# Performance work log

Measured on AMD Instinct MI355X. Metric: run time of the kernel, lower is better.

The kernel has to match this reference:

```python
import jax, jax.numpy as jnp
import numpy as np
import math

HID = 1024      # opt.hidden_dim
NH = 8          # num_heads (hardcoded in module)
HD = HID // NH  # indiv_head_dim = 128
G = 16          # opt.group_num
GD = HID // G   # per-group dim = 64
FEAT = 1024     # opt.feature_dim
V, T = 8, 256   # videos x frames
E = 256         # number of events
L = 64          # max_att_len (clip window)
N = 384         # expanded event_num
WAVE = 10000.0


def setup_inputs() -> dict:
    rng = np.random.RandomState(0)
    key = jax.random.key(0)
    ks = jax.random.split(key, 12)

    feats = jax.random.normal(ks[0], (V * T, FEAT), dtype=jnp.float32)

    # ragged clip spans -> dense gather idx + mask (the Basic_Encoder loop)
    starts = rng.randint(0, V * T - L, size=(E,))
    clip_gather_idx = jnp.asarray(starts[:, None] + np.arange(L)[None, :], dtype=jnp.int32)
    lens = rng.randint(8, L + 1, size=(E,))
    clip_mask = jnp.asarray((np.arange(L)[None, :] < lens[:, None]).astype(np.float32))

    # event_seq_idx expansion: rows -> event ids, block-diagonal mask
    expand_idx = jnp.asarray(rng.randint(0, E, size=(N,)), dtype=jnp.int32)
    block_mask = np.zeros((N, N), dtype=np.float32)
    pos = 0
    while pos < N:
        b = min(int(rng.randint(8, 49)), N - pos)
        block_mask[pos:pos + b, pos:pos + b] = 1.0
        pos += b
    block_mask = jnp.asarray(block_mask)

    # normalized timestamps (start < end, in [0,1])
    s = rng.uniform(0.0, 0.8, size=(N, 1)).astype(np.float32)
    e = s + rng.uniform(0.02, 0.2, size=(N, 1)).astype(np.float32)
    bbox = jnp.asarray(np.concatenate([s, e], axis=1))

    sc = 1.0 / math.sqrt(HID)
    scd = 1.0 / math.sqrt(HD)
    Wpre = jax.random.normal(ks[1], (HID, FEAT), dtype=jnp.float32) * sc
    bpre = jnp.zeros((HID,), dtype=jnp.float32)
    Wq = jax.random.normal(ks[2], (NH, HD, HD), dtype=jnp.float32) * scd
    bq = jnp.zeros((NH, HD), dtype=jnp.float32)
    Wk = jax.random.normal(ks[3], (NH, HD, HD), dtype=jnp.float32) * scd
    bk = jnp.zeros((NH, HD), dtype=jnp.float32)
    Wv = jax.random.normal(ks[4], (NH, HD, HD), dtype=jnp.float32) * scd
    bv = jnp.zeros((NH, HD), dtype=jnp.float32)
    Wp1 = jax.random.normal(ks[5], (HID, HID), dtype=jnp.float32) * sc
    bp1 = jnp.zeros((HID,), dtype=jnp.float32)
    Wp2 = jax.random.normal(ks[6], (G, HID), dtype=jnp.float32) * sc
    bp2 = jnp.zeros((G,), dtype=jnp.float32)

    return dict(feats=feats, clip_gather_idx=clip_gather_idx, clip_mask=clip_mask,
                expand_idx=expand_idx, block_mask=block_mask, bbox=bbox,
                Wpre=Wpre, bpre=bpre, Wq=Wq, bq=bq, Wk=Wk, bk=bk, Wv=Wv, bv=bv,
                Wp1=Wp1, bp1=bp1, Wp2=Wp2, bp2=bp2)


def _sinusoid(x, feat_dim):
    # extract_position_embedding: x [..., P] -> [..., P*feat_dim/2*2] reshaped to feat_dim per row
    fr = jnp.arange(feat_dim // 4, dtype=x.dtype)
    dim_mat = WAVE ** (4.0 / feat_dim * fr)              # (feat_dim/4,)
    div = (100.0 * x)[..., None] / dim_mat               # (..., P, feat_dim/4)
    return jnp.concatenate([jnp.sin(div), jnp.cos(div)], axis=-1)


def reference(feats, clip_gather_idx, clip_mask, expand_idx, block_mask, bbox,
              Wpre, bpre, Wq, bq, Wk, bk, Wv, bv, Wp1, bp1, Wp2, bp2):
    # ---- clip-level pooling (Basic_Encoder.get_clip_level_feats + mean) ----
    clip_feats = feats[clip_gather_idx] * clip_mask[..., None]          # (E, L, FEAT)
    event = clip_feats.sum(1) / (clip_mask.sum(1, keepdims=True) + 1e-5)  # (E, FEAT)
    event = jax.nn.relu(event @ Wpre.T + bpre)                          # pre_map (dropout=eval)

    # ---- expand per event_seq_idx ----
    x = event[expand_idx]                                               # (N, HID)

    # ---- 8 per-head q/k/v maps, split into G groups ----
    xh = x.reshape(N, NH, HD)
    def proj(W, b):
        y = jnp.einsum('nhd,hed->nhe', xh, W) + b                       # (N, NH, HD)
        return y.reshape(N, G, GD).transpose(1, 0, 2)                   # (G, N, GD)
    q, k, v = proj(Wq, bq), proj(Wk, bk), proj(Wv, bv)
    scores = jnp.einsum('gnd,gmd->gnm', q, k) / math.sqrt(GD)           # (G, N, N)

    # ---- position branch: pairwise geometric relation bias ----
    start, end = bbox[:, 0:1], bbox[:, 1:2]                             # (N,1)
    center = 0.5 * (start + end)
    length = jnp.maximum(end - start, 0.1)
    dc = (center - center.T) / length
    dl = jnp.log(length.T / length)
    pm = jnp.stack([dc, dl], axis=2)                                    # (N, N, 2)
    emb = _sinusoid(pm, HID).reshape(N, N, HID)                         # (N, N, HID)
    pos = jax.nn.relu(emb @ Wp1.T + bp1)                                # pair_pos_fc1
    pos = jax.nn.relu(pos @ Wp2.T + bp2)                                # pair_pos_fc2 -> (N, N, G)
    pos_bias = jnp.log(jnp.clip(pos, 1e-6)).transpose(2, 0, 1)          # (G, N, N)

    scores = scores + pos_bias
    scores = jnp.where(block_mask[None] > 0, scores, -1e9)
    att = jax.nn.softmax(scores, axis=-1)                               # (G, N, N)
    out = jnp.einsum('gnm,gmd->gnd', att, v)                            # (G, N, GD)
    out = out.transpose(1, 0, 2).reshape(N, HID)

    # ---- per-event 100-dim temporal position embedding ----
    e100 = _sinusoid(bbox, 100).reshape(N, 100)

    return jnp.concatenate([x, out, e100], axis=-1)                     # (N, 2*HID + 100)
```

## Files before the change

### kernel.cpp

```cpp
#include <hip/hip_runtime.h>
#include <hip/hip_bf16.h>

typedef unsigned short u16;
typedef _Float16 h16;
typedef __attribute__((ext_vector_type(8))) h16 h8;
typedef __attribute__((ext_vector_type(8))) u16 us8;
typedef __attribute__((ext_vector_type(4))) u16 us4;
typedef __attribute__((ext_vector_type(4))) float f4;

#define DEVFN __device__ __forceinline__

constexpr int kN = 384;
constexpr int kL = 64;
constexpr int kMaxP = kN * 48;
constexpr int kOutCols = 2148;
constexpr float kLoScale = 2048.f;
constexpr float kLoInv = 1.f / 2048.f;

union HU { h16 h; u16 u; };
DEVFN u16 f2h(float f) { HU c; c.h = (h16)f; return c.u; }
DEVFN float h2f(u16 b) { HU c; c.u = b; return (float)c.h; }

DEVFN f4 mfma16h(h8 a, h8 b, f4 c) {
  return __builtin_amdgcn_mfma_f32_16x16x32_f16(a, b, c, 0, 0, 0);
}

DEVFN h8 pack8h(float4 x0, float4 x1) {
  h8 a;
  a[0] = (h16)x0.x; a[1] = (h16)x0.y; a[2] = (h16)x0.z; a[3] = (h16)x0.w;
  a[4] = (h16)x1.x; a[5] = (h16)x1.y; a[6] = (h16)x1.z; a[7] = (h16)x1.w;
  return a;
}

DEVFN void fsincos(float ang, float& s, float& c) {
  float n = rintf(ang * 0.15915494309189535f);
  const float PI2_HI = 6.2831854820251465f;
  const float PI2_LO = -1.7484555e-07f;
  float r = fmaf(-n, PI2_HI, ang);
  r = fmaf(-n, PI2_LO, r);
  s = __sinf(r);
  c = __cosf(r);
}

__global__ __launch_bounds__(256) void k_front(
    const float* __restrict__ Wp1, u16* __restrict__ W1H, u16* __restrict__ W1L,
    const float* __restrict__ Wp2, u16* __restrict__ W2H, u16* __restrict__ W2L,
    const float* __restrict__ Wpre, u16* __restrict__ WpreH,
    const float* __restrict__ Wq, u16* __restrict__ WqH,
    const float* __restrict__ Wk, u16* __restrict__ WkH,
    const float* __restrict__ Wv, u16* __restrict__ WvH,
    const float* __restrict__ bm, int* __restrict__ row_start, int* __restrict__ row_len,
    const float* __restrict__ feats, const int* __restrict__ gidx,
    const float* __restrict__ cmask, float* __restrict__ mean,
    float* __restrict__ bias_acc) {
  int bid = blockIdx.x, t = threadIdx.x;
  if (bid < 512) {
    const int nW1 = 1048576, nW2 = 16384, nPre = 1048576, nQ = 131072;
    const int tot = nW1 + nW2 + nPre + 3 * nQ;
    for (int i = bid * 256 + t; i < tot; i += 512 * 256) {
      if (i < nW1) {
        float x = Wp1[i]; u16 h = f2h(x);
        W1H[i] = h; W1L[i] = f2h((x - h2f(h)) * kLoScale);
      } else if (i < nW1 + nW2) {
        int j = i - nW1; float x = Wp2[j]; u16 h = f2h(x);
        W2H[j] = h; W2L[j] = f2h((x - h2f(h)) * kLoScale);
      } else if (i < nW1 + nW2 + nPre) {
        int j = i - nW1 - nW2; WpreH[j] = f2h(Wpre[j]);
      } else {
        int j = i - nW1 - nW2 - nPre;
        int a = j / nQ, r = j % nQ;
        const float* s = (a == 0) ? Wq : (a == 1) ? Wk : Wv;
        u16* d = (a == 0) ? WqH : (a == 1) ? WkH : WvH;
        d[r] = f2h(s[r]);
      }
    }
  } else if (bid < 608) {
    int w = t >> 6, lane = t & 63;
    int i = (bid - 512) * 4 + w;
    int mn = kN, mx = -1;
    #pragma unroll
    for (int jb = 0; jb < kN; jb += 64) {
      float m = bm[(size_t)i * kN + jb + lane];
      if (m > 0.f) { mn = min(mn, jb + lane); mx = max(mx, jb + lane); }
    }
    #pragma unroll
    for (int off = 32; off > 0; off >>= 1) {
      mn = min(mn, __shfl_xor(mn, off));
      mx = max(mx, __shfl_xor(mx, off));
    }
    if (lane == 0) { row_start[i] = mn; row_len[i] = mx - mn + 1; }
  } else if (bid < 864) {
    int e = bid - 608;
    float4 a = {0.f, 0.f, 0.f, 0.f};
    float ms = 0.f;
    for (int l = 0; l < kL; ++l) {
      float m = cmask[e * kL + l];
      ms += m;
      if (m > 0.f) {
        float4 v = *(const float4*)(feats + (size_t)gidx[e * kL + l] * 1024 + t * 4);
        a.x += v.x; a.y += v.y; a.z += v.z; a.w += v.w;
      }
    }
    float inv = 1.f / (ms + 1e-5f);
    float4 o = {a.x * inv, a.y * inv, a.z * inv, a.w * inv};
    *(float4*)(mean + (size_t)e * 1024 + t * 4) = o;
  } else {
    float4 z = {0.f, 0.f, 0.f, 0.f};
    for (int i4 = (bid - 864) * 256 + t; i4 < kMaxP * 16 / 4; i4 += 48 * 256)
      *(float4*)(bias_acc + (size_t)i4 * 4) = z;
  }
}

__global__ __launch_bounds__(64) void k_scan(const int* __restrict__ row_len,
                                             int* __restrict__ row_off,
                                             int* __restrict__ Ptr) {
  int lane = threadIdx.x;
  int s[6], tot = 0;
  #pragma unroll
  for (int r = 0; r < 6; ++r) { s[r] = tot; tot += row_len[lane * 6 + r]; }
  int run = tot;
  #pragma unroll
  for (int off = 1; off < 64; off <<= 1) {
    int u = __shfl_up(run, off);
    if (lane >= off) run += u;
  }
  int excl = run - tot;
  #pragma unroll
  for (int r = 0; r < 6; ++r) row_off[lane * 6 + r] = excl + s[r];
  if (lane == 63) Ptr[0] = excl + tot;
}

__global__ __launch_bounds__(64) void k_fill(const int* __restrict__ row_start,
                                             const int* __restrict__ row_len,
                                             const int* __restrict__ row_off,
                                             int* __restrict__ pair_i,
                                             int* __restrict__ pair_j) {
  int i = blockIdx.x, lane = threadIdx.x;
  int s = row_start[i], len = row_len[i], off = row_off[i];
  if (lane < len) { pair_i[off + lane] = i; pair_j[off + lane] = s + lane; }
}

__global__ __launch_bounds__(256) void k_mid(
    const int* __restrict__ Ptr, const int* __restrict__ row_start,
    const int* __restrict__ row_off, const float* __restrict__ bbox,
    u16* __restrict__ ehi, u16* __restrict__ elo,
    const float* __restrict__ mean, const u16* __restrict__ WpreH,
    const float* __restrict__ bpre, float* __restrict__ event) {
  int bid = blockIdx.x, t = threadIdx.x;
  if (bid < 9216) {
    int P = Ptr[0];
    int Pc = (P + 127) & ~127;
    if (bid * 2 >= Pc) return;
    __shared__ double As[16], Bs[16];
    __shared__ int roff[384], rstart[384];
    const double kCd = -13.287712379549449 / 256.0;
    if (t < 16) As[t] = exp2(kCd * (double)(t * 16));
    else if (t < 32) Bs[t - 16] = exp2(kCd * (double)(t - 16));
    for (int k = t; k < 384; k += 256) { roff[k] = row_off[k]; rstart[k] = row_start[k]; }
    __syncthreads();
    int p = bid * 2 + (t >> 7);
    int u = t & 127;
    int hseg = u >> 6;
    int f0 = (u & 63) * 4;
    size_t ob = (size_t)p * 1024 + hseg * 512 + f0;
    if (p >= P) {
      us4 z = {0, 0, 0, 0};
      *(us4*)(ehi + ob) = z; *(us4*)(ehi + ob + 256) = z;
      *(us4*)(elo + ob) = z; *(us4*)(elo + ob + 256) = z;
      return;
    }
    int lo = 0, hi = 383;
    while (lo < hi) { int md = (lo + hi + 1) >> 1; if (roff[md] <= p) lo = md; else hi = md - 1; }
    int pi = lo, pj = rstart[lo] + (p - roff[lo]);
    double s0 = bbox[pi * 2], e0 = bbox[pi * 2 + 1];
    double s1 = bbox[pj * 2], e1 = bbox[pj * 2 + 1];
    double li = fmax(e0 - s0, 0.1), lj = fmax(e1 - s1, 0.1);
    double x = hseg ? log(lj / li) : (0.5 * (s0 + e0) - 0.5 * (s1 + e1)) / li;
    double x100 = 100.0 * x;
    const double INV2PI = 0.15915494309189535;
    const double TWOPI  = 6.283185307179586;
    us4 sh_, sl_, ch_, cl_;
    #pragma unroll
    for (int j = 0; j < 4; ++j) {
      int f = f0 + j;
      double ang = x100 * (As[f >> 4] * Bs[f & 15]);
      double nn = rint(ang * INV2PI);
      float rf = (float)fma(-nn, TWOPI, ang);
      float sv = __sinf(rf), cv = __cosf(rf);
      u16 hs = f2h(sv); sh_[j] = hs; sl_[j] = f2h((sv - h2f(hs)) * kLoScale);
      u16 hc = f2h(cv); ch_[j] = hc; cl_[j] = f2h((cv - h2f(hc)) * kLoScale);
    }
    *(us4*)(ehi + ob) = sh_; *(us4*)(ehi + ob + 256) = ch_;
    *(us4*)(elo + ob) = sl_; *(us4*)(elo + ob + 256) = cl_;
  } else {
    int b2 = bid - 9216;
    int mt = b2 >> 4, nc = b2 & 15;
    int w = t >> 6, lane = t & 63, lr = lane & 15, lg = lane >> 4;
    f4 acc = {};
    const float* arow = mean + (size_t)(mt * 16 + lr) * 1024;
    #pragma unroll
    for (int ks = 0; ks < 32; ++ks) {
      const float* ap = arow + ks * 32 + lg * 8;
      h8 a = pack8h(*(const float4*)ap, *(const float4*)(ap + 4));
      h8 b = *(const h8*)(WpreH + (size_t)(nc * 64 + w * 16 + lr) * 1024 + ks * 32 + lg * 8);
      acc = mfma16h(a, b, acc);
    }
    #pragma unroll
    for (int r = 0; r < 4; ++r) {
      int row = mt * 16 + lg * 4 + r, cn = nc * 64 + w * 16 + lr;
      event[(size_t)row * 1024 + cn] = fmaxf(acc[r] + bpre[cn], 0.f);
    }
  }
}

__global__ __launch_bounds__(256, 2) void k_main(
    const int* __restrict__ Ptr, const u16* __restrict__ ehi, const u16* __restrict__ elo,
    const u16* __restrict__ W1h, const u16* __restrict__ W1l, const float* __restrict__ bias1,
    const u16* __restrict__ W2h, const u16* __restrict__ W2l, float* __restrict__ bias_acc,
    const float* __restrict__ event, const int* __restrict__ eidx,
    const u16* __restrict__ WqH, const float* __restrict__ bq,
    const u16* __restrict__ WkH, const float* __restrict__ bk,
    const u16* __restrict__ WvH, const float* __restrict__ bv,
    float* __restrict__ qb, float* __restrict__ kbuf, float* __restrict__ vbuf,
    int pos_on) {
  __shared__ u16 lds[2][4][4096];
  int bid = blockIdx.x, tid = threadIdx.x;
  if (bid < 1152) {
    if (!pos_on) return;
    int P = Ptr[0];
    int mb = bid % 144, nb = bid / 144;
    if (mb * 128 >= P) return;
    int w = tid >> 6, lane = tid & 63;
    int lr = lane & 15, lg = lane >> 4;
    int srow[2], scol[2];
    #pragma unroll
    for (int cc = 0; cc < 2; ++cc) {
      int c = w * 2 + cc;
      int d = c * 1024 + lane * 16;
      int b = d ^ (((((d >> 6) & 3)) ^ ((d >> 8) & 3)) << 4);
      srow[cc] = b >> 6;
      scol[cc] = b & 63;
    }
    const u16* planes[4] = {ehi, elo, W1h, W1l};
    int rb0 = mb * 128, rb1 = nb * 128;
    auto stage = [&](int buf, int k0) {
      #pragma unroll
      for (int t = 0; t < 4; ++t) {
        int rbase = (t < 2) ? rb0 : rb1;
        #pragma unroll
        for (int cc = 0; cc < 2; ++cc) {
          int c = w * 2 + cc;
          const char* src = (const char*)(planes[t] + (size_t)(rbase + srow[cc]) * 1024 + k0) + scol[cc];
          char* dst = (char*)&lds[buf][t][0] + c * 1024;
          __builtin_amdgcn_global_load_lds(
              (const __attribute__((address_space(1))) char*)src,
              (__attribute__((address_space(3))) char*)dst, 16, 0, 0);
        }
      }
    };
    stage(0, 0);
    f4 aH[4][4] = {}, aL[4][4] = {};
    int wm = (w >> 1) * 64, wn = (w & 1) * 64;
    int sl = (lg ^ (lr & 3) ^ ((lr >> 2) & 3)) << 4;
    __syncthreads();
    for (int kt = 0; kt < 32; ++kt) {
      int cur = kt & 1;
      if (kt < 31) stage(cur ^ 1, (kt + 1) * 32);
      h8 ah[4], al[4], bh[4], bl[4];
      #pragma unroll
      for (int mt = 0; mt < 4; ++mt) {
        int ad = (wm + mt * 16 + lr) * 64 + sl;
        ah[mt] = *(const h8*)((const char*)&lds[cur][0][0] + ad);
        al[mt] = *(const h8*)((const char*)&lds[cur][1][0] + ad);
      }
      #pragma unroll
      for (int nt = 0; nt < 4; ++nt) {
        int ad = (wn + nt * 16 + lr) * 64 + sl;
        bh[nt] = *(const h8*)((const char*)&lds[cur][2][0] + ad);
        bl[nt] = *(const h8*)((const char*)&lds[cur][3][0] + ad);
      }
      #pragma unroll
      for (int mt = 0; mt < 4; ++mt)
        #pragma unroll
        for (int nt = 0; nt < 4; ++nt) {
          aH[mt][nt] = mfma16h(ah[mt], bh[nt], aH[mt][nt]);
          aL[mt][nt] = mfma16h(al[mt], bh[nt], aL[mt][nt]);
          aL[mt][nt] = mfma16h(ah[mt], bl[nt], aL[mt][nt]);
        }
      __syncthreads();
    }
    float* zq = (float*)&lds[0][0][0] + w * 4096;
    #pragma unroll
    for (int mt = 0; mt < 4; ++mt)
      #pragma unroll
      for (int nt = 0; nt < 4; ++nt)
        #pragma unroll
        for (int r = 0; r < 4; ++r) {
          int pl = mt * 16 + lg * 4 + r;
          int nl = nt * 16 + lr;
          float z1 = aH[mt][nt][r] + aL[mt][nt][r] * kLoInv + bias1[nb * 128 + wn + nl];
          zq[pl * 64 + (nl ^ ((pl & 7) << 3))] = fmaxf(z1, 0.f);
        }
    __syncthreads();
    f4 c2h[4], c2l[4];
    #pragma unroll
    for (int i = 0; i < 4; ++i) { c2h[i] = f4{}; c2l[i] = f4{}; }
    #pragma unroll
    for (int mt2 = 0; mt2 < 4; ++mt2) {
      #pragma unroll
      for (int kc = 0; kc < 2; ++kc) {
        int pl = mt2 * 16 + lr;
        int n0 = kc * 32 + lg * 8;
        const float* rp = zq + pl * 64 + (n0 ^ ((pl & 7) << 3));
        float4 v0 = *(const float4*)rp;
        float4 v1 = *(const float4*)(rp + 4);
        h8 ah2, al2;
        #pragma unroll
        for (int j = 0; j < 4; ++j) {
          h16 h0 = (h16)v0[j]; ah2[j] = h0;     al2[j] = (h16)((v0[j] - (float)h0) * kLoScale);
          h16 h1 = (h16)v1[j]; ah2[4 + j] = h1; al2[4 + j] = (h16)((v1[j] - (float)h1) * kLoScale);
        }
        int ng = nb * 128 + wn + n0;
        h8 bh2 = *(const h8*)(W2h + lr * 1024 + ng);
        h8 bl2 = *(const h8*)(W2l + lr * 1024 + ng);
        c2h[mt2] = mfma16h(ah2, bh2, c2h[mt2]);
        c2l[mt2] = mfma16h(al2, bh2, c2l[mt2]);
        c2l[mt2] = mfma16h(ah2, bl2, c2l[mt2]);
      }
    }
    #pragma unroll
    for (int mt2 = 0; mt2 < 4; ++mt2)
      #pragma unroll
      for (int r = 0; r < 4; ++r) {
        int p = mb * 128 + wm + mt2 * 16 + lg * 4 + r;
        if (p < P)
          atomicAdd(&bias_acc[(size_t)p * 16 + lr], c2h[mt2][r] + c2l[mt2][r] * kLoInv);
      }
  } else {
    int b2 = bid - 1152;
    int z = b2 / 192, r2 = b2 % 192, mt = r2 >> 3, h = r2 & 7;
    int w = tid >> 6, lane = tid & 63, lr = lane & 15, lg = lane >> 4;
    const u16* W = (z == 0) ? WqH : (z == 1) ? WkH : WvH;
    const float* bias = (z == 0) ? bq : (z == 1) ? bk : bv;
    float* out = (z == 0) ? qb : (z == 1) ? kbuf : vbuf;
    int row = mt * 16 + lr;
    const float* arow = event + (size_t)eidx[row] * 1024 + h * 128;
    f4 acc[2] = {};
    #pragma unroll
    for (int ks = 0; ks < 4; ++ks) {
      const float* ap = arow + ks * 32 + lg * 8;
      h8 a = pack8h(*(const float4*)ap, *(const float4*)(ap + 4));
      #pragma unroll
      for (int n2 = 0; n2 < 2; ++n2) {
        int nt = w * 2 + n2;
        h8 b = *(const h8*)(W + h * 16384 + (nt * 16 + lr) * 128 + ks * 32 + lg * 8);
        acc[n2] = mfma16h(a, b, acc[n2]);
      }
    }
    #pragma unroll
    for (int n2 = 0; n2 < 2; ++n2)
      #pragma unroll
      for (int r = 0; r < 4; ++r) {
        int rn = mt * 16 + lg * 4 + r, e = (w * 2 + n2) * 16 + lr;
        out[(size_t)rn * 1024 + h * 128 + e] = acc[n2][r] + bias[h * 128 + e];
      }
  }
}

__global__ __launch_bounds__(64) void k_att(const float* __restrict__ q,
                                            const float* __restrict__ kk,
                                            const float* __restrict__ vv,
                                            const float* __restrict__ bias_acc,
                                            const float* __restrict__ bias2,
                                            const int* __restrict__ row_start,
                                            const int* __restrict__ row_len,
                                            const int* __restrict__ row_off,
                                            const float* __restrict__ event,
                                            const int* __restrict__ eidx,
                                            const float* __restrict__ bbox,
                                            float* __restrict__ dout) {
  int bid = blockIdx.x, lane = threadIdx.x;
  if (bid >= 6144) {
    int i = bid - 6144;
    const float* er = event + (size_t)eidx[i] * 1024;
    float* orow = dout + (size_t)i * kOutCols;
    #pragma unroll
    for (int it = 0; it < 4; ++it) {
      int c = lane * 4 + it * 256;
      *(float4*)(orow + c) = *(const float4*)(er + c);
    }
    for (int t = lane; t < 100; t += 64) {
      int qq = t / 25, f = t % 25;
      float x = bbox[i * 2 + (qq >> 1)];
      float ang = 100.f * x * exp2f((float)f * (-13.287712379549449f * 0.04f));
      float sv, cv;
      fsincos(ang, sv, cv);
      orow[2048 + t] = (qq & 1) ? cv : sv;
    }
    return;
  }
  int i = bid >> 4, g = bid & 15;
  int s = row_start[i], L = row_len[i], pb = row_off[i];
  __shared__ float qs[64];
  __shared__ float att[64];
  qs[lane] = q[(size_t)i * 1024 + g * 64 + lane];
  __syncthreads();
  bool valid = lane < L;
  const float* kr = kk + (size_t)(s + (valid ? lane : 0)) * 1024 + g * 64;
  float sc = 0.f;
  #pragma unroll
  for (int dt = 0; dt < 16; ++dt) {
    float4 kv = *(const float4*)(kr + dt * 4);
    sc += qs[dt * 4 + 0] * kv.x + qs[dt * 4 + 1] * kv.y +
          qs[dt * 4 + 2] * kv.z + qs[dt * 4 + 3] * kv.w;
  }
  int pidx = min(pb + lane, kMaxP - 1);
  float pbias = 0.f;
  if (valid) {
    float zs = bias_acc[(size_t)pidx * 16 + g] + bias2[g];
    pbias = logf(fmaxf(zs, 1e-6f));
  }
  sc = valid ? (sc * 0.125f + pbias) : -3.0e38f;
  float mx = sc;
  #pragma unroll
  for (int off = 32; off > 0; off >>= 1) mx = fmaxf(mx, __shfl_xor(mx, off));
  float pe = valid ? __expf(sc - mx) : 0.f;
  float sm = pe;
  #pragma unroll
  for (int off = 32; off > 0; off >>= 1) sm += __shfl_xor(sm, off);
  att[lane] = pe / sm;
  __syncthreads();
  float o = 0.f;
  const float* vb = vv + (size_t)s * 1024 + g * 64 + lane;
  for (int jl = 0; jl < L; ++jl) o += att[jl] * vb[(size_t)jl * 1024];
  dout[(size_t)i * kOutCols + 1024 + g * 64 + lane] = o;
}

__global__ __launch_bounds__(256) void k_pos(
    const int* __restrict__ Ptr, const int* __restrict__ pair_i,
    const int* __restrict__ pair_j, const float* __restrict__ bbox,
    const u16* __restrict__ W1h, const u16* __restrict__ W1l,
    const float* __restrict__ bias1,
    const u16* __restrict__ W2h, const u16* __restrict__ W2l,
    float* __restrict__ bias_acc) {
  int P = Ptr[0];
  int base0 = blockIdx.x * 64;
  if (base0 >= P) return;
  int w = threadIdx.x >> 6, l = threadIdx.x & 63;
  int lr = l & 15, lg = l >> 4;
  int base = base0 + w * 16;
  int p = base + lr;
  bool valid = p < P;
  int pi = valid ? pair_i[p] : 0;
  int pj = valid ? pair_j[p] : 0;
  double s0 = bbox[pi * 2], e0 = bbox[pi * 2 + 1];
  double s1 = bbox[pj * 2], e1 = bbox[pj * 2 + 1];
  double li = fmax(e0 - s0, 0.1), lj = fmax(e1 - s1, 0.1);
  double dcd = (0.5 * (s0 + e0) - 0.5 * (s1 + e1)) / li;
  double dld = log(lj / li);
  const double kCd = -13.287712379549449 / 256.0;
  double r1  = exp2(kCd);
  double r32 = exp2(kCd * 32.0);
  double pb0 = exp2(kCd * (double)(lg * 8));
  const double INV2PI = 0.15915494309189535;
  const double TWOPI  = 6.283185307179586;
  h8 eh[32], el[32];
  #pragma unroll
  for (int hx = 0; hx < 2; ++hx) {
    double x100 = 100.0 * (hx ? dld : dcd);
    double pch = pb0;
    #pragma unroll
    for (int ksl = 0; ksl < 8; ++ksl) {
      double pp = pch;
      #pragma unroll
      for (int j = 0; j < 8; ++j) {
        double ang = x100 * pp;
        double nn = rint(ang * INV2PI);
        float rf = (float)fma(-nn, TWOPI, ang);
        float sv = __sinf(rf), cv = __cosf(rf);
        h16 sh = (h16)sv, ch = (h16)cv;
        eh[hx * 16 + ksl][j] = sh;
        el[hx * 16 + ksl][j] = (h16)((sv - (float)sh) * kLoScale);
        eh[hx * 16 + 8 + ksl][j] = ch;
        el[hx * 16 + 8 + ksl][j] = (h16)((cv - (float)ch) * kLoScale);
        pp *= r1;
      }
      pch *= r32;
    }
  }
  __shared__ float p1f[4][16 * 64];
  char* myp1 = (char*)p1f[w];
  f4 acc2 = {}, acc2l = {};
  for (int nc = 0; nc < 16; ++nc) {
    f4 accH[4] = {}, accL[4] = {};
    #pragma unroll
    for (int ks = 0; ks < 32; ++ks) {
      #pragma unroll
      for (int nt = 0; nt < 4; ++nt) {
        size_t boff = (size_t)(nc * 64 + nt * 16 + lr) * 1024 + ks * 32 + lg * 8;
        h8 bh = *(const h8*)(W1h + boff);
        h8 bl = *(const h8*)(W1l + boff);
        accH[nt] = mfma16h(eh[ks], bh, accH[nt]);
        accL[nt] = mfma16h(el[ks], bh, accL[nt]);
        accL[nt] = mfma16h(eh[ks], bl, accL[nt]);
      }
    }
    __syncthreads();
    #pragma unroll
    for (int nt = 0; nt < 4; ++nt)
      #pragma unroll
      for (int r = 0; r < 4; ++r) {
        int m = lg * 4 + r, n = nt * 16 + lr;
        float z1 = accH[nt][r] + accL[nt][r] * kLoInv + bias1[nc * 64 + n];
        int byte = ((m * 64 + n) * 4) ^ ((m & 7) << 4);
        *(float*)(myp1 + byte) = fmaxf(z1, 0.f);
      }
    __syncthreads();
    #pragma unroll
    for (int hf = 0; hf < 2; ++hf) {
      int kb = hf * 32 + lg * 8;
      int b0 = ((lr * 64 + kb) * 4) ^ ((lr & 7) << 4);
      int b1 = ((lr * 64 + kb + 4) * 4) ^ ((lr & 7) << 4);
      float4 x0 = *(const float4*)(myp1 + b0);
      float4 x1 = *(const float4*)(myp1 + b1);
      h8 ah, al;
      #pragma unroll
      for (int j = 0; j < 4; ++j) {
        h16 h0 = (h16)x0[j];
        ah[j] = h0; al[j] = (h16)((x0[j] - (float)h0) * kLoScale);
        h16 h1 = (h16)x1[j];
        ah[4 + j] = h1; al[4 + j] = (h16)((x1[j] - (float)h1) * kLoScale);
      }
      h8 bh = *(const h8*)(W2h + lr * 1024 + nc * 64 + kb);
      h8 bl = *(const h8*)(W2l + lr * 1024 + nc * 64 + kb);
      acc2  = mfma16h(ah, bh, acc2);
      acc2l = mfma16h(al, bh, acc2l);
      acc2l = mfma16h(ah, bl, acc2l);
    }
  }
  #pragma unroll
  for (int r = 0; r < 4; ++r) {
    int m = lg * 4 + r;
    int pp = base + m;
    if (pp < P)
      bias_acc[(size_t)pp * 16 + lr] = acc2[r] + acc2l[r] * kLoInv;
  }
}

extern "C" void kernel_launch(void* const* d_in, const int* in_sizes, int n_in,
                              void* d_out, int out_size, void* d_ws, size_t ws_size,
                              hipStream_t stream) {
  const float* feats = (const float*)d_in[0];
  const int*   gidx  = (const int*)d_in[1];
  const float* cmask = (const float*)d_in[2];
  const int*   eidx  = (const int*)d_in[3];
  const float* bmask = (const float*)d_in[4];
  const float* bbox  = (const float*)d_in[5];
  const float* Wpre  = (const float*)d_in[6];
  const float* bpre  = (const float*)d_in[7];
  const float* Wq    = (const float*)d_in[8];
  const float* bq    = (const float*)d_in[9];
  const float* Wk    = (const float*)d_in[10];
  const float* bk    = (const float*)d_in[11];
  const float* Wv    = (const float*)d_in[12];
  const float* bv    = (const float*)d_in[13];
  const float* Wp1   = (const float*)d_in[14];
  const float* bp1   = (const float*)d_in[15];
  const float* Wp2   = (const float*)d_in[16];
  const float* bp2   = (const float*)d_in[17];

  char* ws = (char*)d_ws;
  size_t off = 0;
  auto alloc = [&](size_t bytes) {
    char* r = ws + off;
    off += (bytes + 255) & ~(size_t)255;
    return r;
  };
  u16* W1H   = (u16*)alloc((size_t)1048576 * 2);
  u16* W1L   = (u16*)alloc((size_t)1048576 * 2);
  u16* W2H   = (u16*)alloc((size_t)16384 * 2);
  u16* W2L   = (u16*)alloc((size_t)16384 * 2);
  u16* WpreH = (u16*)alloc((size_t)1048576 * 2);
  u16* WqH   = (u16*)alloc((size_t)131072 * 2);
  u16* WkH   = (u16*)alloc((size_t)131072 * 2);
  u16* WvH   = (u16*)alloc((size_t)131072 * 2);
  float* mean  = (float*)alloc((size_t)256 * 1024 * 4);
  float* event = (float*)alloc((size_t)256 * 1024 * 4);
  float* qb    = (float*)alloc((size_t)384 * 1024 * 4);
  float* kb    = (float*)alloc((size_t)384 * 1024 * 4);
  float* vb    = (float*)alloc((size_t)384 * 1024 * 4);
  int* row_start = (int*)alloc(kN * 4);
  int* row_len   = (int*)alloc(kN * 4);
  int* row_off   = (int*)alloc(kN * 4);
  int* Ptr       = (int*)alloc(256);
  int* pair_i    = (int*)alloc((size_t)kMaxP * 4);
  int* pair_j    = (int*)alloc((size_t)kMaxP * 4);
  float* bias_acc = (float*)alloc((size_t)kMaxP * 16 * 4);
  u16* ehi      = (u16*)alloc((size_t)kMaxP * 1024 * 2);
  u16* elo      = (u16*)alloc((size_t)kMaxP * 1024 * 2);
  bool fast = (off <= ws_size);

  k_front<<<912, 256, 0, stream>>>(Wp1, W1H, W1L, Wp2, W2H, W2L, Wpre, WpreH,
                                   Wq, WqH, Wk, WkH, Wv, WvH,
                                   bmask, row_start, row_len,
                                   feats, gidx, cmask, mean, bias_acc);
  k_scan<<<1, 64, 0, stream>>>(row_len, row_off, Ptr);

  if (fast) {
    k_mid<<<9472, 256, 0, stream>>>(Ptr, row_start, row_off, bbox, ehi, elo,
                                    mean, WpreH, bpre, event);
    k_main<<<1728, 256, 0, stream>>>(Ptr, ehi, elo, W1H, W1L, bp1, W2H, W2L, bias_acc,
                                     event, eidx, WqH, bq, WkH, bk, WvH, bv, qb, kb, vb, 1);
  } else {
    k_mid<<<9472, 256, 0, stream>>>(Ptr, row_start, row_off, bbox, ehi, elo,
                                    mean, WpreH, bpre, event);
    k_fill<<<kN, 64, 0, stream>>>(row_start, row_len, row_off, pair_i, pair_j);
    k_pos<<<kMaxP / 64, 256, 0, stream>>>(Ptr, pair_i, pair_j, bbox, W1H, W1L, bp1,
                                          W2H, W2L, bias_acc);
    k_main<<<1728, 256, 0, stream>>>(Ptr, ehi, elo, W1H, W1L, bp1, W2H, W2L, bias_acc,
                                     event, eidx, WqH, bq, WkH, bk, WvH, bv, qb, kb, vb, 0);
  }
  k_att<<<6528, 64, 0, stream>>>(qb, kb, vb, bias_acc, bp2, row_start, row_len, row_off,
                                 event, eidx, bbox, (float*)d_out);
}
```

Measured before the change: 161.3 us.

## Regroup front kernels so embedding generation overlaps weight conversion

Moves the block-mask extent scan into its own small kernel that runs, together with the prefix scan, before the large front kernel. The pair-embedding generation then joins the weight conversion, clip mean and bias zeroing in one big launch. The event GEMM, which needs the clip means, becomes a separate kernel afterwards. The aim is to run the memory-bound weight conversion alongside the sinusoid embedding work instead of one after the other. In exchange the small row-extent scan now sits serially on the critical path ahead of the big kernel, and there is one extra launch.

```diff
diff --git a/kernel.cpp b/kernel.cpp
--- a/kernel.cpp
+++ b/kernel.cpp
@@ -4,7 +4,6 @@
 typedef unsigned short u16;
 typedef _Float16 h16;
 typedef __attribute__((ext_vector_type(8))) h16 h8;
-typedef __attribute__((ext_vector_type(8))) u16 us8;
 typedef __attribute__((ext_vector_type(4))) u16 us4;
 typedef __attribute__((ext_vector_type(4))) float f4;
 
@@ -42,17 +41,66 @@
   c = __cosf(r);
 }
 
-__global__ __launch_bounds__(256) void k_front(
+__global__ __launch_bounds__(64) void k_ext(const float* __restrict__ bm,
+                                            int* __restrict__ row_start,
+                                            int* __restrict__ row_len) {
+  int i = blockIdx.x, lane = threadIdx.x;
+  int mn = kN, mx = -1;
+  #pragma unroll
+  for (int jb = 0; jb < kN; jb += 64) {
+    float m = bm[(size_t)i * kN + jb + lane];
+    if (m > 0.f) { mn = min(mn, jb + lane); mx = max(mx, jb + lane); }
+  }
+  #pragma unroll
+  for (int off = 32; off > 0; off >>= 1) {
+    mn = min(mn, __shfl_xor(mn, off));
+    mx = max(mx, __shfl_xor(mx, off));
+  }
+  if (lane == 0) { row_start[i] = mn; row_len[i] = mx - mn + 1; }
+}
+
+__global__ __launch_bounds__(64) void k_scan(const int* __restrict__ row_len,
+                                             int* __restrict__ row_off,
+                                             int* __restrict__ Ptr) {
+  int lane = threadIdx.x;
+  int s[6], tot = 0;
+  #pragma unroll
+  for (int r = 0; r < 6; ++r) { s[r] = tot; tot += row_len[lane * 6 + r]; }
+  int run = tot;
+  #pragma unroll
+  for (int off = 1; off < 64; off <<= 1) {
+    int u = __shfl_up(run, off);
+    if (lane >= off) run += u;
+  }
+  int excl = run - tot;
+  #pragma unroll
+  for (int r = 0; r < 6; ++r) row_off[lane * 6 + r] = excl + s[r];
+  if (lane == 63) Ptr[0] = excl + tot;
+}
+
+__global__ __launch_bounds__(64) void k_fill(const int* __restrict__ row_start,
+                                             const int* __restrict__ row_len,
+                                             const int* __restrict__ row_off,
+                                             int* __restrict__ pair_i,
+                                             int* __restrict__ pair_j) {
+  int i = blockIdx.x, lane = threadIdx.x;
+  int s = row_start[i], len = row_len[i], off = row_off[i];
+  if (lane < len) { pair_i[off + lane] = i; pair_j[off + lane] = s + lane; }
+}
+
+__global__ __launch_bounds__(256) void k_big(
     const float* __restrict__ Wp1, u16* __restrict__ W1H, u16* __restrict__ W1L,
     const float* __restrict__ Wp2, u16* __restrict__ W2H, u16* __restrict__ W2L,
     const float* __restrict__ Wpre, u16* __restrict__ WpreH,
     const float* __restrict__ Wq, u16* __restrict__ WqH,
     const float* __restrict__ Wk, u16* __restrict__ WkH,
     const float* __restrict__ Wv, u16* __restrict__ WvH,
-    const float* __restrict__ bm, int* __restrict__ row_start, int* __restrict__ row_len,
     const float* __restrict__ feats, const int* __restrict__ gidx,
     const float* __restrict__ cmask, float* __restrict__ mean,
-    float* __restrict__ bias_acc) {
+    float* __restrict__ bias_acc,
+    const int* __restrict__ Ptr, const int* __restrict__ row_start,
+    const int* __restrict__ row_off, const float* __restrict__ bbox,
+    u16* __restrict__ ehi, u16* __restrict__ elo) {
   int bid = blockIdx.x, t = threadIdx.x;
   if (bid < 512) {
     const int nW1 = 1048576, nW2 = 16384, nPre = 1048576, nQ = 131072;
@@ -74,23 +122,8 @@
         d[r] = f2h(s[r]);
       }
     }
-  } else if (bid < 608) {
-    int w = t >> 6, lane = t & 63;
-    int i = (bid - 512) * 4 + w;
-    int mn = kN, mx = -1;
-    #pragma unroll
-    for (int jb = 0; jb < kN; jb += 64) {
-      float m = bm[(size_t)i * kN + jb + lane];
-      if (m > 0.f) { mn = min(mn, jb + lane); mx = max(mx, jb + lane); }
-    }
-    #pragma unroll
-    for (int off = 32; off > 0; off >>= 1) {
-      mn = min(mn, __shfl_xor(mn, off));
-      mx = max(mx, __shfl_xor(mx, off));
-    }
-    if (lane == 0) { row_start[i] = mn; row_len[i] = mx - mn + 1; }
-  } else if (bid < 864) {
-    int e = bid - 608;
+  } else if (bid < 768) {
+    int e = bid - 512;
     float4 a = {0.f, 0.f, 0.f, 0.f};
     float ms = 0.f;
     for (int l = 0; l < kL; ++l) {
@@ -104,53 +137,15 @@
     float inv = 1.f / (ms + 1e-5f);
     float4 o = {a.x * inv, a.y * inv, a.z * inv, a.w * inv};
     *(float4*)(mean + (size_t)e * 1024 + t * 4) = o;
+  } else if (bid < 816) {
+    float4 z = {0.f, 0.f, 0.f, 0.f};
+    for (int i4 = (bid - 768) * 256 + t; i4 < kMaxP * 16 / 4; i4 += 48 * 256)
+      *(float4*)(bias_acc + (size_t)i4 * 4) = z;
   } else {
-    float4 z = {0.f, 0.f, 0.f, 0.f};
-    for (int i4 = (bid - 864) * 256 + t; i4 < kMaxP * 16 / 4; i4 += 48 * 256)
-      *(float4*)(bias_acc + (size_t)i4 * 4) = z;
-  }
-}
-
-__global__ __launch_bounds__(64) void k_scan(const int* __restrict__ row_len,
-                                             int* __restrict__ row_off,
-                                             int* __restrict__ Ptr) {
-  int lane = threadIdx.x;
-  int s[6], tot = 0;
-  #pragma unroll
-  for (int r = 0; r < 6; ++r) { s[r] = tot; tot += row_len[lane * 6 + r]; }
-  int run = tot;
-  #pragma unroll
-  for (int off = 1; off < 64; off <<= 1) {
-    int u = __shfl_up(run, off);
-    if (lane >= off) run += u;
-  }
-  int excl = run - tot;
-  #pragma unroll
-  for (int r = 0; r < 6; ++r) row_off[lane * 6 + r] = excl + s[r];
-  if (lane == 63) Ptr[0] = excl + tot;
-}
-
-__global__ __launch_bounds__(64) void k_fill(const int* __restrict__ row_start,
-                                             const int* __restrict__ row_len,
-                                             const int* __restrict__ row_off,
-                                             int* __restrict__ pair_i,
-                                             int* __restrict__ pair_j) {
-  int i = blockIdx.x, lane = threadIdx.x;
-  int s = row_start[i], len = row_len[i], off = row_off[i];
-  if (lane < len) { pair_i[off + lane] = i; pair_j[off + lane] = s + lane; }
-}
-
-__global__ __launch_bounds__(256) void k_mid(
-    const int* __restrict__ Ptr, const int* __restrict__ row_start,
-    const int* __restrict__ row_off, const float* __restrict__ bbox,
-    u16* __restrict__ ehi, u16* __restrict__ elo,
-    const float* __restrict__ mean, const u16* __restrict__ WpreH,
-    const float* __restrict__ bpre, float* __restrict__ event) {
-  int bid = blockIdx.x, t = threadIdx.x;
-  if (bid < 9216) {
+    int eb = bid - 816;
     int P = Ptr[0];
     int Pc = (P + 127) & ~127;
-    if (bid * 2 >= Pc) return;
+    if (eb * 2 >= Pc) return;
     __shared__ double As[16], Bs[16];
     __shared__ int roff[384], rstart[384];
     const double kCd = -13.287712379549449 / 256.0;
@@ -158,7 +153,7 @@
     else if (t < 32) Bs[t - 16] = exp2(kCd * (double)(t - 16));
     for (int k = t; k < 384; k += 256) { roff[k] = row_off[k]; rstart[k] = row_start[k]; }
     __syncthreads();
-    int p = bid * 2 + (t >> 7);
+    int p = eb * 2 + (t >> 7);
     int u = t & 127;
     int hseg = u >> 6;
     int f0 = (u & 63) * 4;
@@ -192,24 +187,29 @@
     }
     *(us4*)(ehi + ob) = sh_; *(us4*)(ehi + ob + 256) = ch_;
     *(us4*)(elo + ob) = sl_; *(us4*)(elo + ob + 256) = cl_;
-  } else {
-    int b2 = bid - 9216;
-    int mt = b2 >> 4, nc = b2 & 15;
-    int w = t >> 6, lane = t & 63, lr = lane & 15, lg = lane >> 4;
-    f4 acc = {};
-    const float* arow = mean + (size_t)(mt * 16 + lr) * 1024;
-    #pragma unroll
-    for (int ks = 0; ks < 32; ++ks) {
-      const float* ap = arow + ks * 32 + lg * 8;
-      h8 a = pack8h(*(const float4*)ap, *(const float4*)(ap + 4));
-      h8 b = *(const h8*)(WpreH + (size_t)(nc * 64 + w * 16 + lr) * 1024 + ks * 32 + lg * 8);
-      acc = mfma16h(a, b, acc);
-    }
-    #pragma unroll
-    for (int r = 0; r < 4; ++r) {
-      int row = mt * 16 + lg * 4 + r, cn = nc * 64 + w * 16 + lr;
-      event[(size_t)row * 1024 + cn] = fmaxf(acc[r] + bpre[cn], 0.f);
-    }
+  }
+}
+
+__global__ __launch_bounds__(256) void k_egemm(const float* __restrict__ mean,
+                                               const u16* __restrict__ WpreH,
+                                               const float* __restrict__ bpre,
+                                               float* __restrict__ event) {
+  int mt = blockIdx.x >> 4, nc = blockIdx.x & 15;
+  int t = threadIdx.x;
+  int w = t >> 6, lane = t & 63, lr = lane & 15, lg = lane >> 4;
+  f4 acc = {};
+  const float* arow = mean + (size_t)(mt * 16 + lr) * 1024;
+  #pragma unroll
+  for (int ks = 0; ks < 32; ++ks) {
+    const float* ap = arow + ks * 32 + lg * 8;
+    h8 a = pack8h(*(const float4*)ap, *(const float4*)(ap + 4));
+    h8 b = *(const h8*)(WpreH + (size_t)(nc * 64 + w * 16 + lr) * 1024 + ks * 32 + lg * 8);
+    acc = mfma16h(a, b, acc);
+  }
+  #pragma unroll
+  for (int r = 0; r < 4; ++r) {
+    int row = mt * 16 + lg * 4 + r, cn = nc * 64 + w * 16 + lr;
+    event[(size_t)row * 1024 + cn] = fmaxf(acc[r] + bpre[cn], 0.f);
   }
 }
 
@@ -600,25 +600,25 @@
   u16* elo      = (u16*)alloc((size_t)kMaxP * 1024 * 2);
   bool fast = (off <= ws_size);
 
-  k_front<<<912, 256, 0, stream>>>(Wp1, W1H, W1L, Wp2, W2H, W2L, Wpre, WpreH,
+  k_ext<<<kN, 64, 0, stream>>>(bmask, row_start, row_len);
+  k_scan<<<1, 64, 0, stream>>>(row_len, row_off, Ptr);
+  k_big<<<10032, 256, 0, stream>>>(Wp1, W1H, W1L, Wp2, W2H, W2L, Wpre, WpreH,
                                    Wq, WqH, Wk, WkH, Wv, WvH,
-                                   bmask, row_start, row_len,
-                                   feats, gidx, cmask, mean, bias_acc);
-  k_scan<<<1, 64, 0, stream>>>(row_len, row_off, Ptr);
+                                   feats, gidx, cmask, mean, bias_acc,
+                                   Ptr, row_start, row_off, bbox, ehi, elo);
+  k_egemm<<<256, 256, 0, stream>>>(mean, WpreH, bpre, event);
 
   if (fast) {
-    k_mid<<<9472, 256, 0, stream>>>(Ptr, row_start, row_off, bbox, ehi, elo,
-                                    mean, WpreH, bpre, event);
     k_main<<<1728, 256, 0, stream>>>(Ptr, ehi, elo, W1H, W1L, bp1, W2H, W2L, bias_acc,
-                                     event, eidx, WqH, bq, WkH, bk, WvH, bv, qb, kb, vb, 1);
+                                     event, eidx, WqH, bq, WkH, bk, WvH, bv,
+                                     qb, kb, vb, 1);
   } else {
-    k_mid<<<9472, 256, 0, stream>>>(Ptr, row_start, row_off, bbox, ehi, elo,
-                                    mean, WpreH, bpre, event);
     k_fill<<<kN, 64, 0, stream>>>(row_start, row_len, row_off, pair_i, pair_j);
     k_pos<<<kMaxP / 64, 256, 0, stream>>>(Ptr, pair_i, pair_j, bbox, W1H, W1L, bp1,
                                           W2H, W2L, bias_acc);
     k_main<<<1728, 256, 0, stream>>>(Ptr, ehi, elo, W1H, W1L, bp1, W2H, W2L, bias_acc,
-                                     event, eidx, WqH, bq, WkH, bk, WvH, bv, qb, kb, vb, 0);
+                                     event, eidx, WqH, bq, WkH, bk, WvH, bv,
+                                     qb, kb, vb, 0);
   }
   k_att<<<6528, 64, 0, stream>>>(qb, kb, vb, bias_acc, bp2, row_start, row_len, row_off,
                                  event, eidx, bbox, (float*)d_out);
```

Result: faster. 156.0 us (-3.3%).
